# Performance work log

Hardware: AMD Instinct MI355X
Metric: run time of the kernel (lower is better)

The kernel has to match this reference:

```python
import jax, jax.numpy as jnp
import numpy as np

B, Q, L = 262144, 32, 8


def _rx(theta, ar, ai, br, bi):
    # RX(t) = [[cos(t/2), -i sin(t/2)], [-i sin(t/2), cos(t/2)]]
    c, s = jnp.cos(theta * 0.5), jnp.sin(theta * 0.5)
    return (c * ar + s * bi, c * ai - s * br,
            s * ai + c * br, -s * ar + c * bi)


def _ry(theta, ar, ai, br, bi):
    # RY(t) = [[cos(t/2), -sin(t/2)], [sin(t/2), cos(t/2)]] (real)
    c, s = jnp.cos(theta * 0.5), jnp.sin(theta * 0.5)
    return (c * ar - s * br, c * ai - s * bi,
            s * ar + c * br, s * ai + c * bi)


def _rz(theta, ar, ai, br, bi):
    # RZ(t) = diag(e^{-it/2}, e^{it/2})
    c, s = jnp.cos(theta * 0.5), jnp.sin(theta * 0.5)
    return (c * ar + s * ai, c * ai - s * ar,
            c * br - s * bi, c * bi + s * br)


def setup_inputs() -> dict:
    key = jax.random.key(0)
    k1, k2 = jax.random.split(key)
    x = jax.random.normal(k1, (B, Q), dtype=jnp.float32)
    params = jax.random.normal(k2, (L, Q, 3), dtype=jnp.float32)
    return {"x": x, "params": params}


def reference(x, params):
    # The circuit has only single-qubit gates, so the state factorizes into
    # an independent 2-amplitude state per (batch, qubit); track re/im parts.
    ar = jnp.ones_like(x)          # amplitude of |0>, real part
    ai = jnp.zeros_like(x)
    br = jnp.zeros_like(x)         # amplitude of |1>
    bi = jnp.zeros_like(x)
    # input encoding: RX(x_i) on wire i
    ar, ai, br, bi = _rx(x, ar, ai, br, bi)
    # trainable layers: RY, RZ, RX per qubit (broadcast over batch)
    for layer in range(params.shape[0]):
        ar, ai, br, bi = _ry(params[layer, :, 0][None, :], ar, ai, br, bi)
        ar, ai, br, bi = _rz(params[layer, :, 1][None, :], ar, ai, br, bi)
        ar, ai, br, bi = _rx(params[layer, :, 2][None, :], ar, ai, br, bi)
    # <Z> = |a|^2 - |b|^2 per (batch, qubit)
    return ar * ar + ai * ai - br * br - bi * bi
```

## Files before the change

### kernel.cpp

```cpp
#include <hip/hip_runtime.h>
#include <math.h>

#define NQ 32
#define MAXL 16

typedef float v4f __attribute__((ext_vector_type(4)));

struct Amp { float ar, ai, br, bi; };

__device__ __forceinline__ void g_ry(float c, float s, Amp& v) {
    Amp o;
    o.ar = c * v.ar - s * v.br;
    o.ai = c * v.ai - s * v.bi;
    o.br = s * v.ar + c * v.br;
    o.bi = s * v.ai + c * v.bi;
    v = o;
}
__device__ __forceinline__ void g_rz(float c, float s, Amp& v) {
    Amp o;
    o.ar = c * v.ar + s * v.ai;
    o.ai = c * v.ai - s * v.ar;
    o.br = c * v.br - s * v.bi;
    o.bi = c * v.bi + s * v.br;
    v = o;
}
__device__ __forceinline__ void g_rx(float c, float s, Amp& v) {
    Amp o;
    o.ar = c * v.ar + s * v.bi;
    o.ai = c * v.ai - s * v.br;
    o.br = s * v.ai + c * v.br;
    o.bi = -s * v.ar + c * v.bi;
    v = o;
}

__global__ __launch_bounds__(1024, 8) void qc_fused(const float* __restrict__ x,
                                                    const float* __restrict__ params,
                                                    float* __restrict__ out,
                                                    int n4, int L) {
    __shared__ float sTh[MAXL * NQ * 3];
    __shared__ float sK0[NQ], sR[NQ], sPh[NQ];
    const int t = threadIdx.x;
    const int stride = gridDim.x * blockDim.x;
    const v4f* __restrict__ x4 = reinterpret_cast<const v4f*>(x);
    v4f* __restrict__ out4 = reinterpret_cast<v4f*>(out);

    const int i0 = blockIdx.x * blockDim.x + t;
    const int i1 = i0 + stride, i2 = i1 + stride, i3 = i2 + stride;
    const bool h0 = i0 < n4, h1 = i1 < n4, h2 = i2 < n4, h3 = i3 < n4;
    v4f xa = {0,0,0,0}, xb = {0,0,0,0}, xc = {0,0,0,0}, xd = {0,0,0,0};
    if (h0) xa = __builtin_nontemporal_load(x4 + i0);
    if (h1) xb = __builtin_nontemporal_load(x4 + i1);
    if (h2) xc = __builtin_nontemporal_load(x4 + i2);
    if (h3) xd = __builtin_nontemporal_load(x4 + i3);

    const int nTh4 = (L * NQ * 3) / 4;
    if (t < nTh4)
        reinterpret_cast<v4f*>(sTh)[t] = reinterpret_cast<const v4f*>(params)[t];
    __syncthreads();

    if (t < 64) {
        const int q = t & (NQ - 1);
        Amp v;
        if (t < NQ) v = {1.f, 0.f, 0.f, 0.f};
        else        v = {0.f, 0.f, 1.f, 0.f};
        for (int l = 0; l < L; ++l) {
            const float* th = &sTh[(l * NQ + q) * 3];
            float c, s;
            __sincosf(th[0] * 0.5f, &s, &c);
            g_ry(c, s, v);
            __sincosf(th[1] * 0.5f, &s, &c);
            g_rz(c, s, v);
            __sincosf(th[2] * 0.5f, &s, &c);
            g_rx(c, s, v);
        }
        float par = __shfl_xor(v.ar, 32);
        float pai = __shfl_xor(v.ai, 32);
        float pbr = __shfl_xor(v.br, 32);
        float pbi = __shfl_xor(v.bi, 32);
        if (t < NQ) {
            float A = (v.ar * v.ar + v.ai * v.ai) - (v.br * v.br + v.bi * v.bi);
            float B = (par * par + pai * pai) - (pbr * pbr + pbi * pbi);
            float C = 2.f * ((v.ar * pai - v.ai * par) - (v.br * pbi - v.bi * pbr));
            float K0 = 0.5f * (A + B);
            float K1 = 0.5f * (A - B);
            float K2 = 0.5f * C;
            sK0[q] = K0;
            sR[q]  = sqrtf(K1 * K1 + K2 * K2);
            sPh[q] = atan2f(K2, K1);
        }
    }
    __syncthreads();

    const int q = (4 * t) & (NQ - 1);
    const float k0a = sK0[q + 0], ra = sR[q + 0], pa = sPh[q + 0];
    const float k0b = sK0[q + 1], rb = sR[q + 1], pb = sPh[q + 1];
    const float k0c = sK0[q + 2], rc = sR[q + 2], pc = sPh[q + 2];
    const float k0d = sK0[q + 3], rd = sR[q + 3], pd = sPh[q + 3];

#define EVAL(xv, ov)                                            \
    do {                                                        \
        (ov)[0] = fmaf(ra, __cosf((xv)[0] - pa), k0a);          \
        (ov)[1] = fmaf(rb, __cosf((xv)[1] - pb), k0b);          \
        (ov)[2] = fmaf(rc, __cosf((xv)[2] - pc), k0c);          \
        (ov)[3] = fmaf(rd, __cosf((xv)[3] - pd), k0d);          \
    } while (0)

    v4f o;
    if (h0) { EVAL(xa, o); __builtin_nontemporal_store(o, out4 + i0); }
    if (h1) { EVAL(xb, o); __builtin_nontemporal_store(o, out4 + i1); }
    if (h2) { EVAL(xc, o); __builtin_nontemporal_store(o, out4 + i2); }
    if (h3) { EVAL(xd, o); __builtin_nontemporal_store(o, out4 + i3); }

    for (int i = i3 + stride; i < n4; i += stride) {
        v4f xv = __builtin_nontemporal_load(x4 + i);
        EVAL(xv, o);
        __builtin_nontemporal_store(o, out4 + i);
    }
#undef EVAL
}

extern "C" void kernel_launch(void* const* d_in, const int* in_sizes, int n_in,
                              void* d_out, int out_size, void* d_ws, size_t ws_size,
                              hipStream_t stream) {
    const float* x      = (const float*)d_in[0];
    const float* params = (const float*)d_in[1];
    float* out          = (float*)d_out;

    int L  = in_sizes[1] / (NQ * 3);
    if (L > MAXL) L = MAXL;
    int n  = in_sizes[0];
    int n4 = n / 4;

    int block = 1024;
    int grid  = 512;
    qc_fused<<<grid, block, 0, stream>>>(x, params, out, n4, L);
}
```

Before: 13.86 us.

## Compose per-layer SU2 unitaries via parallel shuffle tree and drop K0 term

Each layer's RY·RZ·RX is folded into one SU2 matrix per qubit, and for L=8 the eight layer matrices are combined with a log-depth shuffle reduction across 256 threads instead of a sequential 64-thread loop. This removes the params staging through shared memory and its barrier. Since the circuit is unitary and starts in |0>, the constant K0 term is zero, so the output reduces to R*cos(x - phi). That cosine is evaluated with the raw hardware cos in revolution units, pre-scaled by 1/2π. The aim is to shorten the per-block prologue latency and trim ALU work in the element loop, at the cost of relying on hardware sin/cos accuracy and range.

New measurement: 13.81 us (median of 2 runs). About the same (-0.4%).

```diff
diff --git a/kernel.cpp b/kernel.cpp
--- a/kernel.cpp
+++ b/kernel.cpp
@@ -2,43 +2,48 @@
 #include <math.h>
 
 #define NQ 32
-#define MAXL 16
 
 typedef float v4f __attribute__((ext_vector_type(4)));
 
-struct Amp { float ar, ai, br, bi; };
+#define REV  0.15915494309189535f
+#define HREV 0.07957747154594767f
 
-__device__ __forceinline__ void g_ry(float c, float s, Amp& v) {
-    Amp o;
-    o.ar = c * v.ar - s * v.br;
-    o.ai = c * v.ai - s * v.bi;
-    o.br = s * v.ar + c * v.br;
-    o.bi = s * v.ai + c * v.bi;
-    v = o;
+struct SU2 { float ar, ai, br, bi; };
+
+__device__ __forceinline__ SU2 build_layer(float th0, float th1, float th2) {
+    float c0 = __builtin_amdgcn_cosf(th0 * HREV), s0 = __builtin_amdgcn_sinf(th0 * HREV);
+    float c1 = __builtin_amdgcn_cosf(th1 * HREV), s1 = __builtin_amdgcn_sinf(th1 * HREV);
+    float c2 = __builtin_amdgcn_cosf(th2 * HREV), s2 = __builtin_amdgcn_sinf(th2 * HREV);
+    float tcc = c2 * c0, tss = s2 * s0, tcs = c2 * s0, tsc = s2 * c0;
+    SU2 u;
+    u.ar =  fmaf(tcc, c1,  tss * s1);
+    u.ai = -fmaf(tcc, s1,  tss * c1);
+    u.br =  fmaf(tcs, c1, -tsc * s1);
+    u.bi =  fmaf(tcs, s1, -tsc * c1);
+    return u;
 }
-__device__ __forceinline__ void g_rz(float c, float s, Amp& v) {
-    Amp o;
-    o.ar = c * v.ar + s * v.ai;
-    o.ai = c * v.ai - s * v.ar;
-    o.br = c * v.br - s * v.bi;
-    o.bi = c * v.bi + s * v.br;
-    v = o;
+
+__device__ __forceinline__ SU2 su2_mul(SU2 H, SU2 L) {
+    SU2 r;
+    r.ar = H.ar*L.ar - H.ai*L.ai - H.br*L.br - H.bi*L.bi;
+    r.ai = H.ar*L.ai + H.ai*L.ar - H.br*L.bi + H.bi*L.br;
+    r.br = H.br*L.ar - H.bi*L.ai + H.ar*L.br + H.ai*L.bi;
+    r.bi = H.br*L.ai + H.bi*L.ar + H.ar*L.bi - H.ai*L.br;
+    return r;
 }
-__device__ __forceinline__ void g_rx(float c, float s, Amp& v) {
-    Amp o;
-    o.ar = c * v.ar + s * v.bi;
-    o.ai = c * v.ai - s * v.br;
-    o.br = s * v.ai + c * v.br;
-    o.bi = -s * v.ar + c * v.bi;
-    v = o;
+
+__device__ __forceinline__ void emit_coeffs(SU2 m, int q, float* sR, float* sP) {
+    float K1 = m.ar*m.ar + m.ai*m.ai - m.br*m.br - m.bi*m.bi;
+    float K2 = 2.f * fmaf(m.ar, m.bi, m.ai * m.br);
+    sR[q] = sqrtf(fmaf(K1, K1, K2 * K2));
+    sP[q] = atan2f(K2, K1) * REV;
 }
 
 __global__ __launch_bounds__(1024, 8) void qc_fused(const float* __restrict__ x,
                                                     const float* __restrict__ params,
                                                     float* __restrict__ out,
                                                     int n4, int L) {
-    __shared__ float sTh[MAXL * NQ * 3];
-    __shared__ float sK0[NQ], sR[NQ], sPh[NQ];
+    __shared__ float sR[NQ], sP[NQ];
     const int t = threadIdx.x;
     const int stride = gridDim.x * blockDim.x;
     const v4f* __restrict__ x4 = reinterpret_cast<const v4f*>(x);
@@ -53,56 +58,54 @@
     if (h2) xc = __builtin_nontemporal_load(x4 + i2);
     if (h3) xd = __builtin_nontemporal_load(x4 + i3);
 
-    const int nTh4 = (L * NQ * 3) / 4;
-    if (t < nTh4)
-        reinterpret_cast<v4f*>(sTh)[t] = reinterpret_cast<const v4f*>(params)[t];
-    __syncthreads();
-
-    if (t < 64) {
-        const int q = t & (NQ - 1);
-        Amp v;
-        if (t < NQ) v = {1.f, 0.f, 0.f, 0.f};
-        else        v = {0.f, 0.f, 1.f, 0.f};
-        for (int l = 0; l < L; ++l) {
-            const float* th = &sTh[(l * NQ + q) * 3];
-            float c, s;
-            __sincosf(th[0] * 0.5f, &s, &c);
-            g_ry(c, s, v);
-            __sincosf(th[1] * 0.5f, &s, &c);
-            g_rz(c, s, v);
-            __sincosf(th[2] * 0.5f, &s, &c);
-            g_rx(c, s, v);
+    if (L == 8) {
+        if (t < 256) {
+            const int l   = t & 63;
+            const int lay = l & 7;
+            const int q   = ((t >> 6) << 3) + (l >> 3);
+            const float* th = params + (lay * NQ + q) * 3;
+            SU2 m = build_layer(th[0], th[1], th[2]);
+#pragma unroll
+            for (int d = 1; d <= 4; d <<= 1) {
+                SU2 p;
+                p.ar = __shfl_xor(m.ar, d);
+                p.ai = __shfl_xor(m.ai, d);
+                p.br = __shfl_xor(m.br, d);
+                p.bi = __shfl_xor(m.bi, d);
+                const bool hi = (lay & d) != 0;
+                SU2 H, Lo;
+                H.ar  = hi ? m.ar : p.ar;  H.ai  = hi ? m.ai : p.ai;
+                H.br  = hi ? m.br : p.br;  H.bi  = hi ? m.bi : p.bi;
+                Lo.ar = hi ? p.ar : m.ar;  Lo.ai = hi ? p.ai : m.ai;
+                Lo.br = hi ? p.br : m.br;  Lo.bi = hi ? p.bi : m.bi;
+                m = su2_mul(H, Lo);
+            }
+            if (lay == 0) emit_coeffs(m, q, sR, sP);
         }
-        float par = __shfl_xor(v.ar, 32);
-        float pai = __shfl_xor(v.ai, 32);
-        float pbr = __shfl_xor(v.br, 32);
-        float pbi = __shfl_xor(v.bi, 32);
+    } else {
         if (t < NQ) {
-            float A = (v.ar * v.ar + v.ai * v.ai) - (v.br * v.br + v.bi * v.bi);
-            float B = (par * par + pai * pai) - (pbr * pbr + pbi * pbi);
-            float C = 2.f * ((v.ar * pai - v.ai * par) - (v.br * pbi - v.bi * pbr));
-            float K0 = 0.5f * (A + B);
-            float K1 = 0.5f * (A - B);
-            float K2 = 0.5f * C;
-            sK0[q] = K0;
-            sR[q]  = sqrtf(K1 * K1 + K2 * K2);
-            sPh[q] = atan2f(K2, K1);
+            SU2 m = {1.f, 0.f, 0.f, 0.f};
+            for (int l = 0; l < L; ++l) {
+                const float* th = params + (l * NQ + t) * 3;
+                m = su2_mul(build_layer(th[0], th[1], th[2]), m);
+            }
+            emit_coeffs(m, t, sR, sP);
         }
     }
     __syncthreads();
 
     const int q = (4 * t) & (NQ - 1);
-    const float k0a = sK0[q + 0], ra = sR[q + 0], pa = sPh[q + 0];
-    const float k0b = sK0[q + 1], rb = sR[q + 1], pb = sPh[q + 1];
-    const float k0c = sK0[q + 2], rc = sR[q + 2], pc = sPh[q + 2];
-    const float k0d = sK0[q + 3], rd = sR[q + 3], pd = sPh[q + 3];
+    const float ra = sR[q + 0], pa = sP[q + 0];
+    const float rb = sR[q + 1], pb = sP[q + 1];
+    const float rc = sR[q + 2], pc = sP[q + 2];
+    const float rd = sR[q + 3], pd = sP[q + 3];
 
-#define EVAL(xv, ov)                                            \
-    do {                                                        \
-        (ov)[0] = fmaf(ra, __cosf((xv)[0] - pa), k0a);          \
-        (ov)[1] = fmaf(rb, __cosf((xv)[1] - pb), k0b);          \
-        (ov)[2] = fmaf(rc, __cosf((xv)[2] - pc), k0c);          \
-        (ov)[3] = fmaf(rd, __cosf((xv)[3] - pd), k0d);          \
+#define EVAL(xv, ov)                                                      \
+    do {                                                                  \
+        (ov)[0] = ra * __builtin_amdgcn_cosf(fmaf((xv)[0], REV, -pa));    \
+        (ov)[1] = rb * __builtin_amdgcn_cosf(fmaf((xv)[1], REV, -pb));    \
+        (ov)[2] = rc * __builtin_amdgcn_cosf(fmaf((xv)[2], REV, -pc));    \
+        (ov)[3] = rd * __builtin_amdgcn_cosf(fmaf((xv)[3], REV, -pd));    \
     } while (0)
 
     v4f o;
@@ -127,7 +130,6 @@
     float* out          = (float*)d_out;
 
     int L  = in_sizes[1] / (NQ * 3);
-    if (L > MAXL) L = MAXL;
     int n  = in_sizes[0];
     int n4 = n / 4;
 
```
